# Kernel tuning notes

Measured on AMD Instinct MI355X. Metric: run time of the kernel, lower is better.

## Reference

```python
import jax, jax.numpy as jnp
import numpy as np


def conv2d(x, w, pad, groups=1):
    # x: [B,Cin,H,W], w: [Cout,Cin/groups,K,K]
    return jax.lax.conv_general_dilated(
        x, w, (1, 1), [(pad, pad), (pad, pad)],
        dimension_numbers=('NCHW', 'OIHW', 'NCHW'),
        feature_group_count=groups)


def setup_inputs() -> dict:
    key = jax.random.key(0)
    ks = jax.random.split(key, 24)
    B, C, H, W = 16, 512, 32, 128          # batch, encoder_dim, feature map
    Da, Ds, De, Dm = 512, 256, 256, 1024   # att_dim, state_dim, embed_dim, mem_dim
    V, Dmerge = 1000, 512
    K, P = 11, 5
    Din = De + C + Dm                       # GRU input dim = 1792
    s = 0.02
    rn = lambda k, shp, sc=1.0: jax.random.normal(k, shp, jnp.float32) * sc
    return {
        'encode': rn(ks[0], (B, C, H, W)),
        'encode_pro': rn(ks[1], (B, Da, H, W)),
        'encode_mask': jnp.ones((B, 1, H, W), jnp.float32),
        'state': rn(ks[2], (B, Ds)),
        'pre_weight': jax.random.uniform(ks[3], (B, 1, H, W), jnp.float32),
        'cum_weight': jax.random.uniform(ks[4], (B, 1, H, W), jnp.float32),
        'context': rn(ks[5], (B, C)),
        'cond_mem': rn(ks[6], (B, Dm)),
        'cond_weight': jax.random.uniform(ks[7], (B, 2, H, W), jnp.float32),
        'label_id': jax.random.randint(ks[8], (B,), 0, V),
        # ImageAttention params (all bias-free per source)
        'w_wt': rn(ks[9], (Da, 1, K, K), s),
        'w_cwt': rn(ks[10], (Da, 1, K, K), s),
        'w_condwt': rn(ks[11], (2 * Da, 1, K, K), s),   # groups=2
        'w_energy': rn(ks[12], (Da,), s),               # 1x1 conv -> vector
        'w_state': rn(ks[13], (Da, Ds), s),
        'w_ctx': rn(ks[14], (Da, C), s),
        'w_cond': rn(ks[15], (Da, Dm), s),
        # GRU params
        'w_i2s': rn(ks[16], (Ds, Din), s), 'b_i2s': jnp.zeros((Ds,), jnp.float32),
        'w_i2g': rn(ks[17], (2 * Ds, Din), s), 'b_i2g': jnp.zeros((2 * Ds,), jnp.float32),
        'w_s2g': rn(ks[18], (2 * Ds, Ds), s),
        'w_h2h': rn(ks[19], (Ds, Ds), s),
        # Readout params
        'embed_table': rn(ks[20], (V, De), s),
        'w_l1': rn(ks[21], (Dmerge, De + Ds + C), s), 'b_l1': jnp.zeros((Dmerge,), jnp.float32),
        'w_l2': rn(ks[22], (V, Dmerge), s), 'b_l2': jnp.zeros((V,), jnp.float32),
    }


def reference(encode, encode_pro, encode_mask, state, pre_weight, cum_weight,
              context, cond_mem, cond_weight, label_id, w_wt, w_cwt, w_condwt,
              w_energy, w_state, w_ctx, w_cond, w_i2s, b_i2s, w_i2g, b_i2g,
              w_s2g, w_h2h, embed_table, w_l1, b_l1, w_l2, b_l2):
    P = (w_wt.shape[-1] - 1) // 2
    Da = w_energy.shape[0]
    B, C, H, W = encode.shape
    # --- ImageAttention ---
    t_pre = conv2d(pre_weight, w_wt, P)           # [B,Da,H,W]
    t_cum = conv2d(cum_weight, w_cwt, P)          # [B,Da,H,W]
    t_cw = conv2d(cond_weight, w_condwt, P, groups=2)
    t_cw = t_cw.reshape(B, 2, Da, H, W).sum(1)    # [B,Da,H,W]
    st = state @ w_state.T + context @ w_ctx.T + cond_mem @ w_cond.T  # [B,Da]
    concat_info = jnp.tanh(st[:, :, None, None] + t_pre + t_cum + t_cw + encode_pro)
    energies = jnp.einsum('bchw,c->bhw', concat_info, w_energy)
    energies = energies + (encode_mask[:, 0] - 1.0) * 1e8
    att = jax.nn.softmax(energies.reshape(B, H * W), axis=1)
    new_weight = att.reshape(B, 1, H, W)
    new_cum_weight = cum_weight + new_weight
    ctx = jnp.einsum('bchw,bhw->bc', encode, new_weight[:, 0])  # [B,C]
    # --- GRU transition (data = [embed, ctx, cond_mem]) ---
    embed = embed_table[label_id]
    data = jnp.concatenate([embed, ctx, cond_mem], axis=1)
    gate = data @ w_i2g.T + b_i2g + state @ w_s2g.T
    Ds = state.shape[1]
    update_g = jax.nn.sigmoid(gate[:, :Ds])
    reset_g = jax.nn.sigmoid(gate[:, Ds:])
    state_hat = jnp.tanh(data @ w_i2s.T + b_i2s + (state * reset_g) @ w_h2h.T)
    new_state = update_g * state_hat + (1.0 - update_g) * state
    # --- Readout.step ---
    merged = jnp.concatenate([embed, new_state, ctx], axis=1)
    hid = jax.nn.relu(merged @ w_l1.T + b_l1)
    readout = hid @ w_l2.T + b_l2                  # [B,V]
    return readout
```

## Files before the change

kernel.cpp:

```cpp
#include <hip/hip_runtime.h>
#include <math.h>

typedef unsigned short u16;
typedef __bf16 bf16x8 __attribute__((ext_vector_type(8)));
typedef float f32x4 __attribute__((ext_vector_type(4)));

__device__ u16   g_A_pack[16 * 512 * 32];
__device__ float g_st[16 * 512];
__device__ float g_eraw[16 * 4096];
__device__ float g_data[16 * 1792];
__device__ float g_merged[16 * 1024];
__device__ float g_update[16 * 256];
__device__ float g_reset[16 * 256];
__device__ float g_i2s[16 * 256];
__device__ float g_hid[16 * 512];

__device__ __forceinline__ u16 f2bf(float f) {
    unsigned u = __float_as_uint(f);
    u = (u + 0x7FFFu + ((u >> 16) & 1u)) >> 16;
    return (u16)u;
}
__device__ __forceinline__ float bf2f(u16 u) {
    return __uint_as_float(((unsigned)u) << 16);
}
__device__ __forceinline__ float fast_tanh(float x) {
    return 1.0f - 2.0f / (__expf(2.0f * x) + 1.0f);
}
__device__ __forceinline__ float sigmoidf_(float x) {
    return 1.0f / (1.0f + __expf(-x));
}

__global__ void k_pre(const float* __restrict__ w_wt, const float* __restrict__ w_cwt,
                      const float* __restrict__ w_condwt, const float* __restrict__ state,
                      const float* __restrict__ context, const float* __restrict__ cond_mem,
                      const float* __restrict__ w_state, const float* __restrict__ w_ctx,
                      const float* __restrict__ w_cond, const int* __restrict__ label,
                      const float* __restrict__ embed_table) {
    int bid = blockIdx.x;
    if (bid < 1024) {
        int idx = bid * 256 + threadIdx.x;
        int d = idx >> 9, k = idx & 511;
        float f = 0.f;
        if (k < 484) {
            int c = k / 121, rem = k % 121;
            if (c == 0)      f = w_wt[d * 121 + rem];
            else if (c == 1) f = w_cwt[d * 121 + rem];
            else if (c == 2) f = w_condwt[d * 121 + rem];
            else             f = w_condwt[(512 + d) * 121 + rem];
        }
        int ks = k >> 5, kl = k & 31;
        g_A_pack[(ks * 512 + d) * 32 + kl] = f2bf(f);
    } else if (bid < 3072) {
        int wid = ((bid - 1024) * 256 + threadIdx.x) >> 6;
        int lane = threadIdx.x & 63;
        if (wid >= 16 * 512) return;
        int b = wid >> 9, d = wid & 511;
        float acc = 0.f;
        for (int k = lane; k < 256; k += 64)  acc += state[b * 256 + k]    * w_state[d * 256 + k];
        for (int k = lane; k < 512; k += 64)  acc += context[b * 512 + k]  * w_ctx[d * 512 + k];
        for (int k = lane; k < 1024; k += 64) acc += cond_mem[b * 1024 + k] * w_cond[d * 1024 + k];
        for (int off = 32; off; off >>= 1) acc += __shfl_down(acc, off, 64);
        if (lane == 0) g_st[b * 512 + d] = acc;
    } else {
        int b = bid - 3072, tid = threadIdx.x;
        int lbl = label[b];
        float ev = embed_table[lbl * 256 + tid];
        g_data[b * 1792 + tid] = ev;
        g_merged[b * 1024 + tid] = ev;
        for (int k = tid; k < 1024; k += 256)
            g_data[b * 1792 + 768 + k] = cond_mem[b * 1024 + k];
    }
}

__global__ __launch_bounds__(512, 4) void k_conv_energy(
    const float* __restrict__ pre_w, const float* __restrict__ cum_w, const float* __restrict__ cond_w,
    const float* __restrict__ encode_pro, const float* __restrict__ w_energy)
{
    __shared__ __align__(16) u16 src[4][11][76];
    __shared__ __align__(16) u16 bchunk[64][40];
    __shared__ __align__(16) u16 epro_l[512 * 68];

    const int blk = blockIdx.x;
    const int pxh = blk & 1;
    const int h = (blk >> 1) & 31;
    const int b = blk >> 6;
    const int px0 = pxh * 64;

    const int tid = threadIdx.x;
    const int lane = tid & 63, wv = tid >> 6;
    const int lr = lane & 15, lg = lane >> 4;

    {
        const float* epbase = encode_pro + (size_t)b * 512 * 4096 + h * 128 + px0;
#pragma unroll
        for (int i = 0; i < 16; ++i) {
            int o = i * 2048 + tid * 4;
            int r = o >> 6, c = o & 63;
            float4 v = *reinterpret_cast<const float4*>(&epbase[(size_t)r * 4096 + c]);
            ushort4 s;
            s.x = f2bf(v.x); s.y = f2bf(v.y); s.z = f2bf(v.z); s.w = f2bf(v.w);
            *reinterpret_cast<ushort4*>(&epro_l[r * 68 + c]) = s;
        }
    }

#pragma unroll
    for (int it = 0; it < 7; ++it) {
        int t = tid + it * 512;
        if (t < 4 * 11 * 76) {
            int c = t / (11 * 76);
            int rem = t % (11 * 76);
            int i = rem / 76, x = rem % 76;
            int row = h + i - 5, w = px0 - 5 + x;
            u16 v = 0;
            if (x < 74 && row >= 0 && row < 32 && w >= 0 && w < 128) {
                const float* img = (c == 0) ? pre_w + b * 4096
                                 : (c == 1) ? cum_w + b * 4096
                                 : (c == 2) ? cond_w + b * 8192
                                            : cond_w + b * 8192 + 4096;
                v = f2bf(img[row * 128 + w]);
            }
            src[c][i][x] = v;
        }
    }
    __syncthreads();

    const int kl = tid & 31;
    const int n0 = tid >> 5;
#define BUILD(KS)                                                               \
    {                                                                           \
        int kg = (KS) * 32 + kl;                                                \
        int c = 0, i = 0, jj = 0;                                               \
        bool ok = (kg < 484);                                                   \
        if (ok) { c = kg / 121; int r2 = kg % 121; i = r2 / 11; jj = r2 % 11; } \
        _Pragma("unroll")                                                       \
        for (int rep = 0; rep < 4; ++rep) {                                     \
            int n = n0 + rep * 16;                                              \
            bchunk[n][kl] = ok ? src[c][i][n + jj] : (u16)0;                    \
        }                                                                       \
    }

    f32x4 acc[4][4];
#pragma unroll
    for (int mt = 0; mt < 4; ++mt)
#pragma unroll
        for (int nt = 0; nt < 4; ++nt) {
            f32x4 z = {0.f, 0.f, 0.f, 0.f};
            acc[mt][nt] = z;
        }

    BUILD(0);
    __syncthreads();

    for (int ks = 0; ks < 16; ++ks) {
        bf16x8 afr[4];
#pragma unroll
        for (int mt = 0; mt < 4; ++mt) {
            int d = wv * 64 + mt * 16 + lr;
            afr[mt] = *reinterpret_cast<const bf16x8*>(&g_A_pack[(ks * 512 + d) * 32 + lg * 8]);
        }
        bf16x8 bfr[4];
#pragma unroll
        for (int nt = 0; nt < 4; ++nt)
            bfr[nt] = *reinterpret_cast<const bf16x8*>(&bchunk[nt * 16 + lr][lg * 8]);

#pragma unroll
        for (int mt = 0; mt < 4; ++mt)
#pragma unroll
            for (int nt = 0; nt < 4; ++nt)
                acc[mt][nt] = __builtin_amdgcn_mfma_f32_16x16x32_bf16(afr[mt], bfr[nt], acc[mt][nt], 0, 0, 0);
        __syncthreads();
        if (ks < 15) {
            BUILD(ks + 1);
            __syncthreads();
        }
    }
#undef BUILD

    float e[4] = {0.f, 0.f, 0.f, 0.f};
#pragma unroll
    for (int mt = 0; mt < 4; ++mt) {
#pragma unroll
        for (int r = 0; r < 4; ++r) {
            int d = wv * 64 + mt * 16 + lg * 4 + r;
            float stv = g_st[b * 512 + d];
            float wev = w_energy[d];
#pragma unroll
            for (int nt = 0; nt < 4; ++nt) {
                int px = nt * 16 + lr;
                float val = stv + acc[mt][nt][r] + bf2f(epro_l[d * 68 + px]);
                e[nt] += wev * fast_tanh(val);
            }
        }
    }

    float* ered = reinterpret_cast<float*>(&bchunk[0][0]);
    __syncthreads();
#pragma unroll
    for (int nt = 0; nt < 4; ++nt) {
        float v = e[nt];
        v += __shfl_xor(v, 16, 64);
        v += __shfl_xor(v, 32, 64);
        if (lane < 16) ered[wv * 64 + nt * 16 + lane] = v;
    }
    __syncthreads();
    if (tid < 64) {
        float v = 0.f;
#pragma unroll
        for (int w = 0; w < 8; ++w) v += ered[w * 64 + tid];
        g_eraw[b * 4096 + h * 128 + px0 + tid] = v;
    }
}

__global__ __launch_bounds__(256) void k_ctx(const float* __restrict__ encode,
                                             const float* __restrict__ encode_mask) {
    __shared__ float att[4096];
    __shared__ float red[256];

    const int bid = blockIdx.x;
    const int b = bid >> 5;
    const int c0 = (bid & 31) * 16;
    const int tid = threadIdx.x;
    const int lane = tid & 63, wvi = tid >> 6;

    float v[16];
    float mx = -1e30f;
#pragma unroll
    for (int i = 0; i < 16; ++i) {
        int idx = tid + i * 256;
        float ev = g_eraw[b * 4096 + idx] + (encode_mask[b * 4096 + idx] - 1.0f) * 1e8f;
        v[i] = ev; mx = fmaxf(mx, ev);
    }
    red[tid] = mx; __syncthreads();
    for (int s = 128; s; s >>= 1) { if (tid < s) red[tid] = fmaxf(red[tid], red[tid + s]); __syncthreads(); }
    mx = red[0]; __syncthreads();
    float sum = 0.f;
#pragma unroll
    for (int i = 0; i < 16; ++i) { v[i] = __expf(v[i] - mx); sum += v[i]; }
    red[tid] = sum; __syncthreads();
    for (int s = 128; s; s >>= 1) { if (tid < s) red[tid] += red[tid + s]; __syncthreads(); }
    float inv = 1.0f / red[0];
#pragma unroll
    for (int i = 0; i < 16; ++i) att[tid + i * 256] = v[i] * inv;
    __syncthreads();

#pragma unroll
    for (int cc = 0; cc < 4; ++cc) {
        int c = c0 + wvi * 4 + cc;
        const float* e = encode + ((size_t)b * 512 + c) * 4096;
        float acc = 0.f;
#pragma unroll
        for (int it = 0; it < 16; ++it) {
            int base = it * 256 + lane * 4;
            float4 ev = *reinterpret_cast<const float4*>(&e[base]);
            float4 av = *reinterpret_cast<const float4*>(&att[base]);
            acc += ev.x * av.x + ev.y * av.y + ev.z * av.z + ev.w * av.w;
        }
        for (int off = 32; off; off >>= 1) acc += __shfl_down(acc, off, 64);
        if (lane == 0) { g_data[b * 1792 + 256 + c] = acc; g_merged[b * 1024 + 512 + c] = acc; }
    }
}

__global__ void k_e1(const float* __restrict__ state,
                     const float* __restrict__ w_i2g, const float* __restrict__ b_i2g,
                     const float* __restrict__ w_s2g, const float* __restrict__ w_i2s,
                     const float* __restrict__ b_i2s) {
    int wid = (blockIdx.x * blockDim.x + threadIdx.x) >> 6;
    int lane = threadIdx.x & 63;
    if (wid >= 16 * 768) return;
    int b = wid / 768, o = wid % 768;
    const float* dt = g_data + b * 1792;
    float acc = 0.f;
    if (o < 512) {
        const float* wr = w_i2g + o * 1792;
        for (int k = lane; k < 1792; k += 64) acc += dt[k] * wr[k];
        const float* wsg = w_s2g + o * 256;
        for (int k = lane; k < 256; k += 64) acc += state[b * 256 + k] * wsg[k];
    } else {
        const float* wr = w_i2s + (o - 512) * 1792;
        for (int k = lane; k < 1792; k += 64) acc += dt[k] * wr[k];
    }
    for (int off = 32; off; off >>= 1) acc += __shfl_down(acc, off, 64);
    if (lane == 0) {
        if (o < 256)       g_update[b * 256 + o]        = sigmoidf_(acc + b_i2g[o]);
        else if (o < 512)  g_reset[b * 256 + (o - 256)] = sigmoidf_(acc + b_i2g[o]);
        else               g_i2s[b * 256 + (o - 512)]   = acc + b_i2s[o - 512];
    }
}

__global__ void k_e2(const float* __restrict__ state, const float* __restrict__ w_h2h) {
    int wid = (blockIdx.x * blockDim.x + threadIdx.x) >> 6;
    int lane = threadIdx.x & 63;
    if (wid >= 16 * 256) return;
    int b = wid >> 8, d = wid & 255;
    const float* wr = w_h2h + d * 256;
    float acc = 0.f;
    for (int k = lane; k < 256; k += 64)
        acc += state[b * 256 + k] * g_reset[b * 256 + k] * wr[k];
    for (int off = 32; off; off >>= 1) acc += __shfl_down(acc, off, 64);
    if (lane == 0) {
        float sh = fast_tanh(g_i2s[b * 256 + d] + acc);
        float u = g_update[b * 256 + d];
        g_merged[b * 1024 + 256 + d] = u * sh + (1.f - u) * state[b * 256 + d];
    }
}

__global__ void k_e3(const float* __restrict__ w_l1, const float* __restrict__ b_l1) {
    int wid = (blockIdx.x * blockDim.x + threadIdx.x) >> 6;
    int lane = threadIdx.x & 63;
    if (wid >= 16 * 512) return;
    int b = wid >> 9, m = wid & 511;
    const float* mg = g_merged + b * 1024;
    const float* wr = w_l1 + m * 1024;
    float acc = 0.f;
    for (int k = lane; k < 1024; k += 64) acc += mg[k] * wr[k];
    for (int off = 32; off; off >>= 1) acc += __shfl_down(acc, off, 64);
    if (lane == 0) g_hid[b * 512 + m] = fmaxf(acc + b_l1[m], 0.f);
}

__global__ void k_e4(const float* __restrict__ w_l2, const float* __restrict__ b_l2,
                     float* __restrict__ out) {
    int wid = (blockIdx.x * blockDim.x + threadIdx.x) >> 6;
    int lane = threadIdx.x & 63;
    if (wid >= 16 * 1000) return;
    int b = wid / 1000, v = wid % 1000;
    const float* hd = g_hid + b * 512;
    const float* wr = w_l2 + v * 512;
    float acc = 0.f;
    for (int k = lane; k < 512; k += 64) acc += hd[k] * wr[k];
    for (int off = 32; off; off >>= 1) acc += __shfl_down(acc, off, 64);
    if (lane == 0) out[b * 1000 + v] = acc + b_l2[v];
}

extern "C" void kernel_launch(void* const* d_in, const int* in_sizes, int n_in,
                              void* d_out, int out_size, void* d_ws, size_t ws_size,
                              hipStream_t stream) {
    static const int EXP[28] = {
        33554432, 33554432, 65536, 4096, 65536, 65536, 8192, 16384, 131072, 16,
        61952, 61952, 123904, 512, 131072, 262144, 524288, 458752, 256, 917504,
        512, 131072, 65536, 256000, 524288, 512, 512000, 1000};
    if (n_in != 28) return;
    for (int i = 0; i < 28; ++i)
        if (in_sizes[i] != EXP[i]) return;

    const float* encode      = (const float*)d_in[0];
    const float* encode_pro  = (const float*)d_in[1];
    const float* encode_mask = (const float*)d_in[2];
    const float* state       = (const float*)d_in[3];
    const float* pre_weight  = (const float*)d_in[4];
    const float* cum_weight  = (const float*)d_in[5];
    const float* context     = (const float*)d_in[6];
    const float* cond_mem    = (const float*)d_in[7];
    const float* cond_weight = (const float*)d_in[8];
    const int*   label_id    = (const int*)d_in[9];
    const float* w_wt     = (const float*)d_in[10];
    const float* w_cwt    = (const float*)d_in[11];
    const float* w_condwt = (const float*)d_in[12];
    const float* w_energy = (const float*)d_in[13];
    const float* w_state  = (const float*)d_in[14];
    const float* w_ctx    = (const float*)d_in[15];
    const float* w_cond   = (const float*)d_in[16];
    const float* w_i2s    = (const float*)d_in[17];
    const float* b_i2s    = (const float*)d_in[18];
    const float* w_i2g    = (const float*)d_in[19];
    const float* b_i2g    = (const float*)d_in[20];
    const float* w_s2g    = (const float*)d_in[21];
    const float* w_h2h    = (const float*)d_in[22];
    const float* embed_t  = (const float*)d_in[23];
    const float* w_l1     = (const float*)d_in[24];
    const float* b_l1     = (const float*)d_in[25];
    const float* w_l2     = (const float*)d_in[26];
    const float* b_l2     = (const float*)d_in[27];
    float* out = (float*)d_out;
    (void)d_ws; (void)ws_size;

    k_pre<<<3088, 256, 0, stream>>>(w_wt, w_cwt, w_condwt, state, context, cond_mem,
                                    w_state, w_ctx, w_cond, label_id, embed_t);
    k_conv_energy<<<1024, 512, 0, stream>>>(pre_weight, cum_weight, cond_weight,
                                            encode_pro, w_energy);
    k_ctx<<<512, 256, 0, stream>>>(encode, encode_mask);
    k_e1<<<3072, 256, 0, stream>>>(state, w_i2g, b_i2g, w_s2g, w_i2s, b_i2s);
    k_e2<<<1024, 256, 0, stream>>>(state, w_h2h);
    k_e3<<<2048, 256, 0, stream>>>(w_l1, b_l1);
    k_e4<<<4000, 256, 0, stream>>>(w_l2, b_l2, out);
}
```

Before: 161.2 us.

## Split conv-energy kernel across two channel halves with partial energy sums

Each conv-energy block now covers half of the 512 attention channels, which doubles the grid to 2048 blocks and halves the per-block shared memory for encode_pro. This allows higher occupancy (launch bounds raised to 6 blocks per CU). The two partial energy sums are written to separate buffers and added in the softmax kernel. In exchange, the im2col B-chunk build and the source tile loads are duplicated across the two channel halves.

```diff
diff --git a/kernel.cpp b/kernel.cpp
--- a/kernel.cpp
+++ b/kernel.cpp
@@ -7,7 +7,7 @@
 
 __device__ u16   g_A_pack[16 * 512 * 32];
 __device__ float g_st[16 * 512];
-__device__ float g_eraw[16 * 4096];
+__device__ float g_epart[2 * 16 * 4096];
 __device__ float g_data[16 * 1792];
 __device__ float g_merged[16 * 1024];
 __device__ float g_update[16 * 256];
@@ -72,28 +72,31 @@
     }
 }
 
-__global__ __launch_bounds__(512, 4) void k_conv_energy(
+__global__ __launch_bounds__(512, 6) void k_conv_energy(
     const float* __restrict__ pre_w, const float* __restrict__ cum_w, const float* __restrict__ cond_w,
     const float* __restrict__ encode_pro, const float* __restrict__ w_energy)
 {
     __shared__ __align__(16) u16 src[4][11][76];
     __shared__ __align__(16) u16 bchunk[64][40];
-    __shared__ __align__(16) u16 epro_l[512 * 68];
+    __shared__ __align__(16) u16 epro_l[256 * 68];
 
     const int blk = blockIdx.x;
-    const int pxh = blk & 1;
-    const int h = (blk >> 1) & 31;
-    const int b = blk >> 6;
+    const int dh = blk & 1;
+    const int pxh = (blk >> 1) & 1;
+    const int h = (blk >> 2) & 31;
+    const int b = blk >> 7;
     const int px0 = pxh * 64;
+    const int d0 = dh * 256;
 
     const int tid = threadIdx.x;
     const int lane = tid & 63, wv = tid >> 6;
+    const int wm = wv >> 1, wn = wv & 1;
     const int lr = lane & 15, lg = lane >> 4;
 
     {
-        const float* epbase = encode_pro + (size_t)b * 512 * 4096 + h * 128 + px0;
-#pragma unroll
-        for (int i = 0; i < 16; ++i) {
+        const float* epbase = encode_pro + (size_t)(b * 512 + d0) * 4096 + h * 128 + px0;
+#pragma unroll
+        for (int i = 0; i < 8; ++i) {
             int o = i * 2048 + tid * 4;
             int r = o >> 6, c = o & 63;
             float4 v = *reinterpret_cast<const float4*>(&epbase[(size_t)r * 4096 + c]);
@@ -139,11 +142,11 @@
         }                                                                       \
     }
 
-    f32x4 acc[4][4];
+    f32x4 acc[4][2];
 #pragma unroll
     for (int mt = 0; mt < 4; ++mt)
 #pragma unroll
-        for (int nt = 0; nt < 4; ++nt) {
+        for (int nt = 0; nt < 2; ++nt) {
             f32x4 z = {0.f, 0.f, 0.f, 0.f};
             acc[mt][nt] = z;
         }
@@ -155,18 +158,18 @@
         bf16x8 afr[4];
 #pragma unroll
         for (int mt = 0; mt < 4; ++mt) {
-            int d = wv * 64 + mt * 16 + lr;
+            int d = d0 + wm * 64 + mt * 16 + lr;
             afr[mt] = *reinterpret_cast<const bf16x8*>(&g_A_pack[(ks * 512 + d) * 32 + lg * 8]);
         }
-        bf16x8 bfr[4];
-#pragma unroll
-        for (int nt = 0; nt < 4; ++nt)
-            bfr[nt] = *reinterpret_cast<const bf16x8*>(&bchunk[nt * 16 + lr][lg * 8]);
+        bf16x8 bfr[2];
+#pragma unroll
+        for (int nt = 0; nt < 2; ++nt)
+            bfr[nt] = *reinterpret_cast<const bf16x8*>(&bchunk[wn * 32 + nt * 16 + lr][lg * 8]);
 
 #pragma unroll
         for (int mt = 0; mt < 4; ++mt)
 #pragma unroll
-            for (int nt = 0; nt < 4; ++nt)
+            for (int nt = 0; nt < 2; ++nt)
                 acc[mt][nt] = __builtin_amdgcn_mfma_f32_16x16x32_bf16(afr[mt], bfr[nt], acc[mt][nt], 0, 0, 0);
         __syncthreads();
         if (ks < 15) {
@@ -176,18 +179,18 @@
     }
 #undef BUILD
 
-    float e[4] = {0.f, 0.f, 0.f, 0.f};
+    float e[2] = {0.f, 0.f};
 #pragma unroll
     for (int mt = 0; mt < 4; ++mt) {
 #pragma unroll
         for (int r = 0; r < 4; ++r) {
-            int d = wv * 64 + mt * 16 + lg * 4 + r;
-            float stv = g_st[b * 512 + d];
-            float wev = w_energy[d];
-#pragma unroll
-            for (int nt = 0; nt < 4; ++nt) {
-                int px = nt * 16 + lr;
-                float val = stv + acc[mt][nt][r] + bf2f(epro_l[d * 68 + px]);
+            int dl = wm * 64 + mt * 16 + lg * 4 + r;
+            float stv = g_st[b * 512 + d0 + dl];
+            float wev = w_energy[d0 + dl];
+#pragma unroll
+            for (int nt = 0; nt < 2; ++nt) {
+                int px = wn * 32 + nt * 16 + lr;
+                float val = stv + acc[mt][nt][r] + bf2f(epro_l[dl * 68 + px]);
                 e[nt] += wev * fast_tanh(val);
             }
         }
@@ -196,18 +199,19 @@
     float* ered = reinterpret_cast<float*>(&bchunk[0][0]);
     __syncthreads();
 #pragma unroll
-    for (int nt = 0; nt < 4; ++nt) {
+    for (int nt = 0; nt < 2; ++nt) {
         float v = e[nt];
         v += __shfl_xor(v, 16, 64);
         v += __shfl_xor(v, 32, 64);
-        if (lane < 16) ered[wv * 64 + nt * 16 + lane] = v;
+        if (lane < 16) ered[wv * 32 + nt * 16 + lane] = v;
     }
     __syncthreads();
     if (tid < 64) {
+        int wnp = tid >> 5, l = tid & 31;
         float v = 0.f;
 #pragma unroll
-        for (int w = 0; w < 8; ++w) v += ered[w * 64 + tid];
-        g_eraw[b * 4096 + h * 128 + px0 + tid] = v;
+        for (int wmp = 0; wmp < 4; ++wmp) v += ered[(wmp * 2 + wnp) * 32 + l];
+        g_epart[(size_t)dh * 65536 + b * 4096 + h * 128 + px0 + tid] = v;
     }
 }
 
@@ -226,8 +230,9 @@
     float mx = -1e30f;
 #pragma unroll
     for (int i = 0; i < 16; ++i) {
-        int idx = tid + i * 256;
-        float ev = g_eraw[b * 4096 + idx] + (encode_mask[b * 4096 + idx] - 1.0f) * 1e8f;
+        int idx = b * 4096 + tid + i * 256;
+        float ev = g_epart[idx] + g_epart[65536 + idx]
+                 + (encode_mask[idx] - 1.0f) * 1e8f;
         v[i] = ev; mx = fmaxf(mx, ev);
     }
     red[tid] = mx; __syncthreads();
@@ -375,7 +380,7 @@
 
     k_pre<<<3088, 256, 0, stream>>>(w_wt, w_cwt, w_condwt, state, context, cond_mem,
                                     w_state, w_ctx, w_cond, label_id, embed_t);
-    k_conv_energy<<<1024, 512, 0, stream>>>(pre_weight, cum_weight, cond_weight,
+    k_conv_energy<<<2048, 512, 0, stream>>>(pre_weight, cum_weight, cond_weight,
                                             encode_pro, w_energy);
     k_ctx<<<512, 256, 0, stream>>>(encode, encode_mask);
     k_e1<<<3072, 256, 0, stream>>>(state, w_i2g, b_i2g, w_s2g, w_i2s, b_i2s);
```

Result: slower. 185.3 us (+15.0%).
